# Kernel tuning notes

Measured on AMD Instinct MI355X. Metric: run time of the kernel, lower is better.

The kernel has to match this reference:

```python
import jax, jax.numpy as jnp
import numpy as np

D = 1024
B, N = 4, 2048

def setup_inputs() -> dict:
    key = jax.random.key(0)
    ks = jax.random.split(key, 7)
    sc = 1.0 / np.sqrt(D)
    return {
        "x": jax.random.normal(ks[0], (B, N, D), dtype=jnp.float32),
        "wq_w": jax.random.normal(ks[1], (D, D), dtype=jnp.float32) * sc,
        "wq_b": jax.random.normal(ks[2], (D,), dtype=jnp.float32) * 0.01,
        "wk_w": jax.random.normal(ks[3], (D, D), dtype=jnp.float32) * sc,
        "wk_b": jax.random.normal(ks[4], (D,), dtype=jnp.float32) * 0.01,
        "wv_w": jax.random.normal(ks[5], (D, D), dtype=jnp.float32) * sc,
        "wv_b": jax.random.normal(ks[6], (D,), dtype=jnp.float32) * 0.01,
    }

def reference(x, wq_w, wq_b, wk_w, wk_b, wv_w, wv_b):
    # torch Linear: y = x @ W^T + b
    q = x @ wq_w.T + wq_b
    k = x @ wk_w.T + wk_b
    v = x @ wv_w.T + wv_b
    d = q.shape[-1]
    s = jnp.einsum("bid,bjd->bij", q, k) / jnp.sqrt(jnp.float32(d))
    # faithful to original: triu then transpose (zeros, NOT -inf, enter the softmax)
    t = jnp.swapaxes(jnp.triu(s), -2, -1)
    p = jax.nn.softmax(t, axis=-2)
    attn = jnp.swapaxes(jnp.triu(p), -2, -1) @ v
    return attn
```

## Files before the change

kernel.cpp:

```cpp
#include <hip/hip_runtime.h>
#include <hip/hip_fp16.h>
#include <cstdint>

typedef _Float16 half8_t __attribute__((ext_vector_type(8)));
typedef float f32x4 __attribute__((ext_vector_type(4)));

#define D_ 1024
#define B_ 4
#define N_ 2048
#define M_ (B_*N_)
#define NC_ 3072

#define OFF_WCAT  0u
#define OFF_BCAT  6291456u
#define OFF_XB    6303744u
#define OFF_Q     23080960u
#define OFF_K     39858176u
#define OFF_V     56635392u
#define OFF_ZP    73412608u
#define OFF_DEXP  74461184u
#define OFF_SV    74493952u
#define OFF_INVD  74756096u
#define OFF_CD    74788864u

__device__ __forceinline__ void gload_lds16(const void* g, void* l) {
  __builtin_amdgcn_global_load_lds(
      (const __attribute__((address_space(1))) unsigned int*)(uintptr_t)g,
      (__attribute__((address_space(3))) unsigned int*)(uintptr_t)l, 16, 0, 0);
}

__device__ __forceinline__ void stage128x64(const __half* rowbase, char* lds, int tid) {
#pragma unroll
  for (int inst = 0; inst < 4; ++inst) {
    int L  = inst * 4096 + tid * 16;
    int r  = L >> 7;
    int cb = L & 127;
    int cbs = cb ^ ((r & 7) << 4);
    gload_lds16((const char*)rowbase + (size_t)r * (D_ * 2) + cbs, lds + L);
  }
}

__device__ __forceinline__ half8_t ldsfrag(const char* lds, int row, int cbyte) {
  int b = (row << 7) + (cbyte ^ ((row & 7) << 4));
  return *reinterpret_cast<const half8_t*>(lds + b);
}

__device__ __forceinline__ void gemm128_core(const __half* Arow0, const __half* Brow0,
                                             char* As, char* Bs, f32x4 acc[4][4]) {
  const int tid  = threadIdx.x;
  const int lane = tid & 63;
  const int wave = tid >> 6;
  const int wm = wave >> 1, wn = wave & 1;
  for (int kt = 0; kt < 16; ++kt) {
    if (kt) __syncthreads();
    stage128x64(Arow0 + kt * 64, As, tid);
    stage128x64(Brow0 + kt * 64, Bs, tid);
    asm volatile("s_waitcnt vmcnt(0)" ::: "memory");
    __syncthreads();
#pragma unroll
    for (int kk = 0; kk < 2; ++kk) {
      const int cbyte = kk * 64 + (lane >> 4) * 16;
      half8_t a[4], b[4];
#pragma unroll
      for (int mf = 0; mf < 4; ++mf) a[mf] = ldsfrag(As, wm * 64 + mf * 16 + (lane & 15), cbyte);
#pragma unroll
      for (int nf = 0; nf < 4; ++nf) b[nf] = ldsfrag(Bs, wn * 64 + nf * 16 + (lane & 15), cbyte);
#pragma unroll
      for (int mf = 0; mf < 4; ++mf)
#pragma unroll
        for (int nf = 0; nf < 4; ++nf)
          acc[mf][nf] = __builtin_amdgcn_mfma_f32_16x16x32_f16(a[mf], b[nf], acc[mf][nf], 0, 0, 0);
    }
  }
}

__device__ __forceinline__ void calc_soff(int tid, int soff[4]) {
#pragma unroll
  for (int i = 0; i < 4; ++i) {
    int L = i * 8192 + tid * 16;
    int s = L >> 10;
    int w = L & 1023;
    w ^= ((w >> 9) & 1) << 5;
    int r  = (s >> 1) * 16 + (w >> 6);
    int kb = (s & 1) * 64 + (w & 63);
    soff[i] = r * 2048 + kb;
  }
}

#define MFMA_QUAD(QM, QN)                                                     \
  _Pragma("unroll")                                                           \
  for (int ks = 0; ks < 2; ++ks)                                              \
    _Pragma("unroll")                                                         \
    for (int mf = 0; mf < 4; ++mf)                                            \
      _Pragma("unroll")                                                       \
      for (int nf = 0; nf < 2; ++nf)                                          \
        acc[(QM)*4 + mf][(QN)*2 + nf] = __builtin_amdgcn_mfma_f32_16x16x32_f16( \
            a[mf][ks], b[(QN)][nf][ks], acc[(QM)*4 + mf][(QN)*2 + nf], 0, 0, 0);

__device__ __forceinline__ void gemm256_8ph(const char* Ag, const char* Bg,
                                            char* smem, f32x4 acc[8][4]) {
  const int tid  = threadIdx.x;
  const int lane = tid & 63;
  const int wave = tid >> 6;
  const int wm = wave >> 2, wn = wave & 3;

  int soff[4];
  calc_soff(tid, soff);
  const int wlane = (((lane & 15) * 64 + (lane >> 4) * 16)) ^ (((lane >> 3) & 1) << 5);

#pragma unroll
  for (int i = 0; i < 4; ++i) gload_lds16(Ag + soff[i], smem + i * 8192 + tid * 16);
#pragma unroll
  for (int i = 0; i < 4; ++i) gload_lds16(Bg + soff[i], smem + 32768 + i * 8192 + tid * 16);
  asm volatile("s_waitcnt vmcnt(0)" ::: "memory");
  __builtin_amdgcn_s_barrier();

  for (int t = 0; t < 16; ++t) {
    char* A0  = smem + ((t & 1) << 16);
    char* B0  = A0 + 32768;
    char* A1  = smem + (((t + 1) & 1) << 16);
    char* B1s = A1 + 32768;
    const half8_t* ap = (const half8_t*)(A0 + wm * 16384 + wlane);
    const half8_t* bp = (const half8_t*)(B0 + wn * 8192 + wlane);
    const char* Agn = Ag + (t + 1) * 128;
    const char* Bgn = Bg + (t + 1) * 128;
    const bool pre = (t < 15);

    half8_t a[4][2];
    half8_t b[2][2][2];

#pragma unroll
    for (int mf = 0; mf < 4; ++mf)
#pragma unroll
      for (int ks = 0; ks < 2; ++ks)
        a[mf][ks] = ap[(mf * 2 + ks) * 64];
#pragma unroll
    for (int nf = 0; nf < 2; ++nf)
#pragma unroll
      for (int ks = 0; ks < 2; ++ks)
        b[0][nf][ks] = bp[(nf * 2 + ks) * 64];
    if (pre) {
#pragma unroll
      for (int i = 0; i < 4; ++i) gload_lds16(Agn + soff[i], A1 + i * 8192 + tid * 16);
    }
    __builtin_amdgcn_s_barrier();
    asm volatile("s_waitcnt lgkmcnt(0)" ::: "memory");
    __builtin_amdgcn_s_setprio(1);
    MFMA_QUAD(0, 0)
    __builtin_amdgcn_s_setprio(0);
    __builtin_amdgcn_s_barrier();

#pragma unroll
    for (int nf = 0; nf < 2; ++nf)
#pragma unroll
      for (int ks = 0; ks < 2; ++ks)
        b[1][nf][ks] = bp[((2 + nf) * 2 + ks) * 64];
    if (pre) {
#pragma unroll
      for (int i = 0; i < 4; ++i) gload_lds16(Bgn + soff[i], B1s + i * 8192 + tid * 16);
    }
    __builtin_amdgcn_s_barrier();
    asm volatile("s_waitcnt lgkmcnt(0)" ::: "memory");
    __builtin_amdgcn_s_setprio(1);
    MFMA_QUAD(0, 1)
    __builtin_amdgcn_s_setprio(0);
    __builtin_amdgcn_s_barrier();

#pragma unroll
    for (int mf = 0; mf < 4; ++mf)
#pragma unroll
      for (int ks = 0; ks < 2; ++ks)
        a[mf][ks] = ap[((4 + mf) * 2 + ks) * 64];
    __builtin_amdgcn_s_barrier();
    asm volatile("s_waitcnt lgkmcnt(0)" ::: "memory");
    __builtin_amdgcn_s_setprio(1);
    MFMA_QUAD(1, 0)
    __builtin_amdgcn_s_setprio(0);
    __builtin_amdgcn_s_barrier();

    __builtin_amdgcn_s_setprio(1);
    MFMA_QUAD(1, 1)
    __builtin_amdgcn_s_setprio(0);
    if (pre) asm volatile("s_waitcnt vmcnt(0)" ::: "memory");
    __builtin_amdgcn_s_barrier();
  }
}

__global__ __launch_bounds__(256) void k_prep(
    const float* __restrict__ x, const float* __restrict__ wq, const float* __restrict__ wk,
    const float* __restrict__ wv, const float* __restrict__ bq, const float* __restrict__ bk,
    const float* __restrict__ bv, __half* __restrict__ xb, __half* __restrict__ wcat,
    float* __restrict__ bcat, float* __restrict__ Zpart) {
  const int NX4 = (M_ * D_) / 4;
  const int NW4 = (D_ * D_) / 4;
  const int TOT = NX4 + 3 * NW4;
  int tid0 = blockIdx.x * 256 + threadIdx.x;
  int stride = gridDim.x * 256;
  for (int i = tid0; i < TOT; i += stride) {
    float4 f; __half* dst;
    if (i < NX4) {
      f = ((const float4*)x)[i];
      dst = xb + 4 * (size_t)i;
    } else {
      int j = i - NX4; int w = j / NW4; int o = j - w * NW4;
      const float* src = (w == 0) ? wq : (w == 1) ? wk : wv;
      f = ((const float4*)src)[o];
      dst = wcat + (size_t)w * (D_ * D_) + 4 * (size_t)o;
    }
    __half h0 = __float2half(f.x), h1 = __float2half(f.y),
           h2 = __float2half(f.z), h3 = __float2half(f.w);
    ushort4 u = { __half_as_ushort(h0), __half_as_ushort(h1),
                  __half_as_ushort(h2), __half_as_ushort(h3) };
    *((ushort4*)dst) = u;
  }
  if (tid0 < NC_)
    bcat[tid0] = (tid0 < 1024) ? bq[tid0] : (tid0 < 2048) ? bk[tid0 - 1024] : bv[tid0 - 2048];
  for (int i = tid0; i < M_ * 32; i += stride) Zpart[i] = 0.f;
}

__global__ __launch_bounds__(256) void k_qkv(
    const __half* __restrict__ xb, const __half* __restrict__ wcat,
    const float* __restrict__ bcat,
    __half* __restrict__ q, __half* __restrict__ kx, __half* __restrict__ v) {
  __shared__ __align__(16) char smem[32768];
  char* As = smem; char* Bs = smem + 16384;
  int bid = blockIdx.x;
  int bm = bid / 24, bn = bid % 24;
  f32x4 acc[4][4];
#pragma unroll
  for (int i = 0; i < 4; ++i)
#pragma unroll
    for (int j = 0; j < 4; ++j) acc[i][j] = f32x4{0.f, 0.f, 0.f, 0.f};
  gemm128_core(xb + (size_t)bm * 128 * D_, wcat + (size_t)bn * 128 * D_, As, Bs, acc);

  const int lane = threadIdx.x & 63;
  const int wave = threadIdx.x >> 6;
  const int wm = wave >> 1, wn = wave & 1;
  int sel = bn >> 3;
  __half* outp = (sel == 0) ? q : (sel == 1) ? kx : v;
#pragma unroll
  for (int nf = 0; nf < 4; ++nf) {
    int nloc = wn * 64 + nf * 16 + (lane & 15);
    float bias = bcat[bn * 128 + nloc];
    int ncol = (bn & 7) * 128 + nloc;
#pragma unroll
    for (int mf = 0; mf < 4; ++mf) {
#pragma unroll
      for (int r = 0; r < 4; ++r) {
        int m = bm * 128 + wm * 64 + mf * 16 + (lane >> 4) * 4 + r;
        outp[(size_t)m * D_ + ncol] = __float2half(acc[mf][nf][r] + bias);
      }
    }
  }
}

__global__ __launch_bounds__(512, 2) void k_stats256(
    const __half* __restrict__ q, const __half* __restrict__ kx,
    float* __restrict__ Zpart, float* __restrict__ dexp) {
  __shared__ __align__(16) char smem[131072];
  int bid = blockIdx.x;
  int tile = (bid & 7) * 18 + (bid >> 3);
  int b = tile / 36;
  int r = tile % 36;
  int ti = 0;
  while (r >= 8 - ti) { r -= 8 - ti; ++ti; }
  int tj = ti + r;

  f32x4 acc[8][4];
#pragma unroll
  for (int i = 0; i < 8; ++i)
#pragma unroll
    for (int j = 0; j < 4; ++j) acc[i][j] = f32x4{0.f, 0.f, 0.f, 0.f};

  const size_t base = (size_t)b * N_ * D_;
  gemm256_8ph((const char*)(q + base + (size_t)ti * 256 * D_),
              (const char*)(kx + base + (size_t)tj * 256 * D_), smem, acc);

  const int lane = threadIdx.x & 63;
  const int wave = threadIdx.x >> 6;
  const int wm = wave >> 2, wn = wave & 3;
  const bool offd = (tj > ti);
  const float scale = 0.03125f;
  int zr0 = b * N_ + ti * 256;
#pragma unroll
  for (int mf = 0; mf < 8; ++mf) {
#pragma unroll
    for (int rr = 0; rr < 4; ++rr) {
      int il = wm * 128 + mf * 16 + (lane >> 4) * 4 + rr;
      float ssum = 0.f;
#pragma unroll
      for (int nf = 0; nf < 4; ++nf) {
        int jl = wn * 64 + nf * 16 + (lane & 15);
        float e = __expf(acc[mf][nf][rr] * scale);
        bool keep = offd || (jl >= il);
        if (!offd && jl == il) dexp[zr0 + il] = e;
        ssum += keep ? e : 0.f;
      }
      ssum += __shfl_xor(ssum, 1);
      ssum += __shfl_xor(ssum, 2);
      ssum += __shfl_xor(ssum, 4);
      ssum += __shfl_xor(ssum, 8);
      if ((lane & 15) == 0)
        Zpart[(size_t)(zr0 + il) * 32 + tj * 4 + wn] = ssum;
    }
  }
}

__global__ __launch_bounds__(256) void k_mid(
    const __half* __restrict__ v, const float* __restrict__ Zpart,
    const float* __restrict__ dexp, float* __restrict__ Sv,
    float* __restrict__ invD, float* __restrict__ cdiag) {
  int tid = blockIdx.x * 256 + threadIdx.x;
  int b = tid >> 14, c = (tid >> 10) & 15, d = tid & 1023;
  const __half* vp = v + ((size_t)(b * N_ + c * 128)) * D_ + d;
  float s = 0.f;
#pragma unroll 8
  for (int r2 = 0; r2 < 128; ++r2) s += __half2float(vp[(size_t)r2 * D_]);
  Sv[tid] = s;
  if (tid < M_) {
    float z = 0.f;
#pragma unroll
    for (int t = 0; t < 32; ++t) z += Zpart[(size_t)tid * 32 + t];
    float Dd = (float)(tid & (N_ - 1)) + z;
    float iv = 1.f / Dd;
    invD[tid] = iv;
    cdiag[tid] = dexp[tid] * iv;
  }
}

__global__ __launch_bounds__(256) void k_out(
    const __half* __restrict__ v, const float* __restrict__ Sv,
    const float* __restrict__ invD, const float* __restrict__ cdiag,
    float* __restrict__ out) {
  int tid = blockIdx.x * 256 + threadIdx.x;
  int b = tid >> 14, c = (tid >> 10) & 15, d = tid & 1023;
  float run = 0.f;
  for (int cc = 0; cc < c; ++cc) run += Sv[((b << 4) + cc) * 1024 + d];
  const __half* vp = v + ((size_t)(b * N_ + c * 128)) * D_ + d;
  float* op = out + ((size_t)(b * N_ + c * 128)) * D_ + d;
  int zi0 = b * N_ + c * 128;
#pragma unroll 4
  for (int r2 = 0; r2 < 128; ++r2) {
    float vi = __half2float(vp[(size_t)r2 * D_]);
    op[(size_t)r2 * D_] = run * invD[zi0 + r2] + cdiag[zi0 + r2] * vi;
    run += vi;
  }
}

extern "C" void kernel_launch(void* const* d_in, const int* in_sizes, int n_in,
                              void* d_out, int out_size, void* d_ws, size_t ws_size,
                              hipStream_t stream) {
  const float* x  = (const float*)d_in[0];
  const float* wq = (const float*)d_in[1];
  const float* bq = (const float*)d_in[2];
  const float* wk = (const float*)d_in[3];
  const float* bk = (const float*)d_in[4];
  const float* wv = (const float*)d_in[5];
  const float* bv = (const float*)d_in[6];
  float* out = (float*)d_out;
  char* ws = (char*)d_ws;

  __half* wcat = (__half*)(ws + OFF_WCAT);
  float*  bcat = (float*)(ws + OFF_BCAT);
  __half* xb   = (__half*)(ws + OFF_XB);
  __half* q    = (__half*)(ws + OFF_Q);
  __half* k    = (__half*)(ws + OFF_K);
  __half* v    = (__half*)(ws + OFF_V);
  float* Zpart = (float*)(ws + OFF_ZP);
  float* dexp  = (float*)(ws + OFF_DEXP);
  float* Sv    = (float*)(ws + OFF_SV);
  float* invD  = (float*)(ws + OFF_INVD);
  float* cdiag = (float*)(ws + OFF_CD);

  k_prep<<<dim3(2048), dim3(256), 0, stream>>>(x, wq, wk, wv, bq, bk, bv, xb, wcat, bcat, Zpart);
  k_qkv<<<dim3(64 * 24), dim3(256), 0, stream>>>(xb, wcat, bcat, q, k, v);
  k_stats256<<<dim3(144), dim3(512), 0, stream>>>(q, k, Zpart, dexp);
  k_mid<<<dim3(256), dim3(256), 0, stream>>>(v, Zpart, dexp, Sv, invD, cdiag);
  k_out<<<dim3(256), dim3(256), 0, stream>>>(v, Sv, invD, cdiag, out);
}
```

Before: 137.4 us.

## Split V prefix-sum into 32-row slabs with vectorized loads in mid/out kernels

Result: no change. 136.8 us (-0.5%).

```diff
diff --git a/kernel.cpp b/kernel.cpp
--- a/kernel.cpp
+++ b/kernel.cpp
@@ -20,8 +20,8 @@
 #define OFF_ZP    73412608u
 #define OFF_DEXP  74461184u
 #define OFF_SV    74493952u
-#define OFF_INVD  74756096u
-#define OFF_CD    74788864u
+#define OFF_INVD  75542528u
+#define OFF_CD    75575296u
 
 __device__ __forceinline__ void gload_lds16(const void* g, void* l) {
   __builtin_amdgcn_global_load_lds(
@@ -310,17 +310,32 @@
     const __half* __restrict__ v, const float* __restrict__ Zpart,
     const float* __restrict__ dexp, float* __restrict__ Sv,
     float* __restrict__ invD, float* __restrict__ cdiag) {
+  int slab = blockIdx.x;
+  int b = slab >> 6, c = slab & 63;
+  int dg = threadIdx.x;
+  int d0 = dg * 4;
+  const ushort4* vp = (const ushort4*)(v + ((size_t)(b * N_ + c * 32)) * D_ + d0);
+  f32x4 s = {0.f, 0.f, 0.f, 0.f};
+#pragma unroll 8
+  for (int r2 = 0; r2 < 32; ++r2) {
+    ushort4 u = vp[r2 * (D_ / 4)];
+    s[0] += __half2float(__ushort_as_half(u.x));
+    s[1] += __half2float(__ushort_as_half(u.y));
+    s[2] += __half2float(__ushort_as_half(u.z));
+    s[3] += __half2float(__ushort_as_half(u.w));
+  }
+  *(f32x4*)(Sv + (size_t)slab * D_ + d0) = s;
+
   int tid = blockIdx.x * 256 + threadIdx.x;
-  int b = tid >> 14, c = (tid >> 10) & 15, d = tid & 1023;
-  const __half* vp = v + ((size_t)(b * N_ + c * 128)) * D_ + d;
-  float s = 0.f;
-#pragma unroll 8
-  for (int r2 = 0; r2 < 128; ++r2) s += __half2float(vp[(size_t)r2 * D_]);
-  Sv[tid] = s;
   if (tid < M_) {
-    float z = 0.f;
-#pragma unroll
-    for (int t = 0; t < 32; ++t) z += Zpart[(size_t)tid * 32 + t];
+    const f32x4* zp = (const f32x4*)(Zpart + (size_t)tid * 32);
+    f32x4 z4 = {0.f, 0.f, 0.f, 0.f};
+#pragma unroll
+    for (int t = 0; t < 8; ++t) {
+      f32x4 zz = zp[t];
+      z4[0] += zz[0]; z4[1] += zz[1]; z4[2] += zz[2]; z4[3] += zz[3];
+    }
+    float z = z4[0] + z4[1] + z4[2] + z4[3];
     float Dd = (float)(tid & (N_ - 1)) + z;
     float iv = 1.f / Dd;
     invD[tid] = iv;
@@ -332,18 +347,39 @@
     const __half* __restrict__ v, const float* __restrict__ Sv,
     const float* __restrict__ invD, const float* __restrict__ cdiag,
     float* __restrict__ out) {
-  int tid = blockIdx.x * 256 + threadIdx.x;
-  int b = tid >> 14, c = (tid >> 10) & 15, d = tid & 1023;
-  float run = 0.f;
-  for (int cc = 0; cc < c; ++cc) run += Sv[((b << 4) + cc) * 1024 + d];
-  const __half* vp = v + ((size_t)(b * N_ + c * 128)) * D_ + d;
-  float* op = out + ((size_t)(b * N_ + c * 128)) * D_ + d;
-  int zi0 = b * N_ + c * 128;
+  __shared__ float sInv[32], sCd[32];
+  int slab = blockIdx.x;
+  int b = slab >> 6, c = slab & 63;
+  int dg = threadIdx.x;
+  int d0 = dg * 4;
+  int zi0 = b * N_ + c * 32;
+  if (dg < 32) sInv[dg] = invD[zi0 + dg];
+  else if (dg < 64) sCd[dg - 32] = cdiag[zi0 + dg - 32];
+  __syncthreads();
+
+  f32x4 run = {0.f, 0.f, 0.f, 0.f};
+  for (int cc = 0; cc < c; ++cc) {
+    f32x4 sv = *(const f32x4*)(Sv + (size_t)((b << 6) + cc) * D_ + d0);
+    run[0] += sv[0]; run[1] += sv[1]; run[2] += sv[2]; run[3] += sv[3];
+  }
+  const ushort4* vp = (const ushort4*)(v + (size_t)zi0 * D_ + d0);
+  float* op = out + (size_t)zi0 * D_ + d0;
 #pragma unroll 4
-  for (int r2 = 0; r2 < 128; ++r2) {
-    float vi = __half2float(vp[(size_t)r2 * D_]);
-    op[(size_t)r2 * D_] = run * invD[zi0 + r2] + cdiag[zi0 + r2] * vi;
-    run += vi;
+  for (int r2 = 0; r2 < 32; ++r2) {
+    ushort4 u = vp[r2 * (D_ / 4)];
+    f32x4 vi;
+    vi[0] = __half2float(__ushort_as_half(u.x));
+    vi[1] = __half2float(__ushort_as_half(u.y));
+    vi[2] = __half2float(__ushort_as_half(u.z));
+    vi[3] = __half2float(__ushort_as_half(u.w));
+    float iv = sInv[r2], cd = sCd[r2];
+    f32x4 o;
+    o[0] = run[0] * iv + cd * vi[0];
+    o[1] = run[1] * iv + cd * vi[1];
+    o[2] = run[2] * iv + cd * vi[2];
+    o[3] = run[3] * iv + cd * vi[3];
+    *(f32x4*)(op + (size_t)r2 * D_) = o;
+    run[0] += vi[0]; run[1] += vi[1]; run[2] += vi[2]; run[3] += vi[3];
   }
 }
 
```
